# Performance work log

Hardware: AMD Instinct MI355X
Metric: run time of the kernel (lower is better)

## Reference

```python
import jax, jax.numpy as jnp
import numpy as np

# AdaptiveSoftmax.forward (fairseq), no adaptive_inputs, dropout=0 (eval-equivalent).
# cutoff after __init__ appends vocab_size: [10000, 30000, 50000]
CUTOFF = (10000, 30000, 50000)


def setup_inputs() -> dict:
    key = jax.random.key(0)
    ks = jax.random.split(key, 7)
    B, T, D = 2, 2048, 1024
    head_dim = CUTOFF[0] + (len(CUTOFF) - 1)  # 10002
    d0 = int(D // 4.0 ** 1)  # 256
    d1 = int(D // 4.0 ** 2)  # 64
    inp = {
        "input": jax.random.normal(ks[0], (B, T, D), jnp.float32),
        "target": jax.random.randint(ks[1], (B, T), 0, CUTOFF[-1], jnp.int32),
        # xavier-ish scaled params
        "head_w": jax.random.normal(ks[2], (head_dim, D), jnp.float32) * 0.02,
        "proj0_w": jax.random.normal(ks[3], (d0, D), jnp.float32) * 0.04,
        "out0_w": jax.random.normal(ks[4], (CUTOFF[1] - CUTOFF[0], d0), jnp.float32) * 0.02,
        "proj1_w": jax.random.normal(ks[5], (d1, D), jnp.float32) * 0.06,
        "out1_w": jax.random.normal(ks[6], (CUTOFF[2] - CUTOFF[1], d1), jnp.float32) * 0.02,
    }
    return inp


def reference(input, target, head_w, proj0_w, out0_w, proj1_w, out1_w):
    c0, c1, c2 = CUTOFF
    D = input.shape[-1]
    h = input.reshape(-1, D)            # [N, D] (dropout p=0 -> identity)
    t = target.reshape(-1)              # [N]

    # band membership masks (adapt_target routing)
    m0 = (t >= c0) & (t < c1)
    m1 = (t >= c1) & (t < c2)

    # new_target[0]: tail tokens remapped to class slots c0+i
    new_t_head = jnp.where(m0, c0, jnp.where(m1, c0 + 1, t))
    # per-band relative targets (0 for rows not in the band; original returns
    # ragged gathered targets -- here dense+masked equivalent)
    new_t0 = jnp.where(m0, t - c0, 0)
    new_t1 = jnp.where(m1, t - c1, 0)

    # head: Linear(D -> c0 + n_tails, bias=False)
    head_out = jnp.einsum('nd,vd->nv', h, head_w)  # [N, 10002]

    # tails: proj (D->dim) then out (dim->band_size); original applies only to
    # gathered band rows -- dense version masked to zero outside the band
    # computes the same values on band rows.
    tail0 = jnp.einsum('nk,vk->nv', jnp.einsum('nd,kd->nk', h, proj0_w), out0_w)
    tail0 = tail0 * m0[:, None].astype(tail0.dtype)  # [N, 20000]
    tail1 = jnp.einsum('nk,vk->nv', jnp.einsum('nd,kd->nk', h, proj1_w), out1_w)
    tail1 = tail1 * m1[:, None].astype(tail1.dtype)  # [N, 20000]

    return (head_out, tail0, tail1, new_t_head, new_t0, new_t1)
```

## Files before the change

kernel.cpp:

```cpp
#include <hip/hip_runtime.h>

#define C0 10000
#define C1 30000
#define C2 50000

typedef __attribute__((ext_vector_type(8))) short short8;
typedef __attribute__((ext_vector_type(8))) unsigned short ushort8;
typedef __attribute__((ext_vector_type(4))) float f32x4;

__device__ __forceinline__ unsigned short f2bf(float f) {
    unsigned int u = __float_as_uint(f);
    u += 0x7FFF + ((u >> 16) & 1);
    return (unsigned short)(u >> 16);
}

#define SZ_IN    (4096 * 1024)
#define OFF_IN   0
#define HW_ROWSP 10240
#define SZ_HW    (HW_ROWSP * 1024)
#define REAL_HW  (10002 * 1024)
#define OFF_HW   (OFF_IN + SZ_IN)
#define OFF_PJ   (OFF_HW + SZ_HW)
#define SZ_PJ    (512 * 1024)
#define PJ_P0    (256 * 1024)
#define PJ_P1    (64 * 1024)
#define O0_ROWSP 20096
#define SZ_O0    (O0_ROWSP * 256)
#define REAL_O0  (20000 * 256)
#define OFF_O0   (OFF_PJ + SZ_PJ)
#define O1_ROWSP 20096
#define SZ_O1    (O1_ROWSP * 64)
#define REAL_O1  (20000 * 64)
#define OFF_O1   (OFF_O0 + SZ_O0)
#define CVT_TOTAL (OFF_O1 + SZ_O1)
#define OFF_PP0C CVT_TOTAL
#define SZ_PP0C  (4096 * 256)
#define OFF_PP1C (OFF_PP0C + SZ_PP0C)
#define SZ_PP1C  (4096 * 64)
#define OFF_IDX  (OFF_PP1C + SZ_PP1C)

__global__ __launch_bounds__(256) void convert_kernel(
    const float* __restrict__ in,  const float* __restrict__ hw,
    const float* __restrict__ p0w, const float* __restrict__ o0w,
    const float* __restrict__ p1w, const float* __restrict__ o1w,
    unsigned short* __restrict__ ws,
    const int* __restrict__ target,
    float* __restrict__ o3, float* __restrict__ o4, float* __restrict__ o5)
{
    long long tid = (long long)blockIdx.x * blockDim.x + threadIdx.x;
    if (tid < 4096) {
        int tg = target[tid];
        bool m0 = (tg >= C0) && (tg < C1);
        bool m1 = (tg >= C1) && (tg < C2);
        o3[tid] = (float)(m0 ? C0 : (m1 ? (C0 + 1) : tg));
        o4[tid] = (float)(m0 ? (tg - C0) : 0);
        o5[tid] = (float)(m1 ? (tg - C1) : 0);
    }
    long long i = tid * 8;
    if (i >= CVT_TOTAL) return;
    const float* src;
    long long rel, real;
    if (i < OFF_HW)                      { src = in;  rel = i - OFF_IN;            real = SZ_IN;   }
    else if (i < OFF_PJ)                 { src = hw;  rel = i - OFF_HW;            real = REAL_HW; }
    else if (i < OFF_PJ + PJ_P0)         { src = p0w; rel = i - OFF_PJ;            real = PJ_P0;   }
    else if (i < OFF_PJ + PJ_P0 + PJ_P1) { src = p1w; rel = i - (OFF_PJ + PJ_P0);  real = PJ_P1;   }
    else if (i < OFF_O0)                 { src = p1w; rel = 1;                     real = 0;       }
    else if (i < OFF_O1)                 { src = o0w; rel = i - OFF_O0;            real = REAL_O0; }
    else                                 { src = o1w; rel = i - OFF_O1;            real = REAL_O1; }
    ushort8 o;
    if (rel < real) {
        float4 v0 = *(const float4*)(src + rel);
        float4 v1 = *(const float4*)(src + rel + 4);
        o[0] = f2bf(v0.x); o[1] = f2bf(v0.y); o[2] = f2bf(v0.z); o[3] = f2bf(v0.w);
        o[4] = f2bf(v1.x); o[5] = f2bf(v1.y); o[6] = f2bf(v1.z); o[7] = f2bf(v1.w);
    } else {
        o = (ushort8)0;
    }
    *(ushort8*)(ws + i) = o;
}

__global__ __launch_bounds__(1024) void build_idx(const int* __restrict__ target,
                                                  int* __restrict__ idx0,
                                                  int* __restrict__ idx1,
                                                  int* __restrict__ cnts)
{
    __shared__ int wsum0[16], wsum1[16];
    __shared__ int base0, base1;
    const int t = threadIdx.x, lane = t & 63, wv = t >> 6;
    if (t == 0) { base0 = 0; base1 = 0; }
    __syncthreads();
    for (int r = 0; r < 4; r++) {
        int i = r * 1024 + t;
        int tg = target[i];
        bool p0 = (tg >= C0) && (tg < C1);
        bool p1 = (tg >= C1) && (tg < C2);
        unsigned long long b0 = __ballot(p0);
        unsigned long long b1 = __ballot(p1);
        int pre0 = __popcll(b0 & ((1ull << lane) - 1));
        int pre1 = __popcll(b1 & ((1ull << lane) - 1));
        if (lane == 0) { wsum0[wv] = __popcll(b0); wsum1[wv] = __popcll(b1); }
        __syncthreads();
        int woff0 = base0, woff1 = base1;
        for (int k = 0; k < wv; k++) { woff0 += wsum0[k]; woff1 += wsum1[k]; }
        if (p0) idx0[woff0 + pre0] = i;
        if (p1) idx1[woff1 + pre1] = i;
        __syncthreads();
        if (t == 0) {
            for (int k = 0; k < 16; k++) { base0 += wsum0[k]; base1 += wsum1[k]; }
        }
        __syncthreads();
    }
    for (int j = base0 + t; j < 4096; j += 1024) idx0[j] = 0;
    for (int j = base1 + t; j < 4096; j += 1024) idx1[j] = 0;
    if (t == 0) { cnts[0] = base0; cnts[1] = base1; }
}

__global__ __launch_bounds__(256) void fill_nonband(
    const int* __restrict__ target,
    float* __restrict__ tail0, float* __restrict__ tail1)
{
    int row   = blockIdx.x >> 1;
    int which = blockIdx.x & 1;
    int tg = target[row];
    bool in = which ? (tg >= C1 && tg < C2) : (tg >= C0 && tg < C1);
    if (in) return;
    float4* dst = (float4*)((which ? tail1 : tail0) + (size_t)row * 20000);
    float4 z = {0.f, 0.f, 0.f, 0.f};
    for (int i = threadIdx.x; i < 5000; i += 256) dst[i] = z;
}

#define BM 128
#define BN 128
#define BK 64

__global__ __launch_bounds__(256) void proj_gather(
    const unsigned short* __restrict__ A,
    const unsigned short* __restrict__ pjw,
    unsigned short* __restrict__ pp0c, unsigned short* __restrict__ pp1c,
    const int* __restrict__ idx0, const int* __restrict__ idx1,
    const int* __restrict__ cnts)
{
    const int band = blockIdx.z;
    if (band == 1 && blockIdx.x > 0) return;
    const int* idx = band ? idx1 : idx0;
    const int cnt = cnts[band];
    const int mBase = blockIdx.y * BM;
    if (mBase >= cnt) return;
    const unsigned short* B = pjw + (band ? (size_t)PJ_P0 : 0);
    const int Nn = band ? 64 : 256;
    unsigned short* Cb = band ? pp1c : pp0c;
    const int K = 1024;

    __shared__ unsigned short As[BM * BK];
    __shared__ unsigned short Bs[BN * BK];

    const int t    = threadIdx.x;
    const int lane = t & 63;
    const int w    = t >> 6;
    const int wr   = w >> 1;
    const int wc   = w & 1;
    const int nBase = blockIdx.x * BN;
    const int srow = lane >> 3;
    const int scol = (lane & 7) * 8;

    int rowsIdx[4];
    #pragma unroll
    for (int c = 0; c < 4; c++)
        rowsIdx[c] = idx[mBase + w * 32 + c * 8 + srow];

    f32x4 acc[4][4] = {};

    for (int k0 = 0; k0 < K; k0 += BK) {
        #pragma unroll
        for (int c = 0; c < 4; c++) {
            const int rbase = w * 32 + c * 8;
            const unsigned short* ga = A + (size_t)rowsIdx[c] * K + k0 + scol;
            __builtin_amdgcn_global_load_lds(
                (const __attribute__((address_space(1))) void*)ga,
                (__attribute__((address_space(3))) void*)&As[rbase * BK], 16, 0, 0);
            const unsigned short* gb = B + (size_t)(nBase + rbase + srow) * K + k0 + scol;
            __builtin_amdgcn_global_load_lds(
                (const __attribute__((address_space(1))) void*)gb,
                (__attribute__((address_space(3))) void*)&Bs[rbase * BK], 16, 0, 0);
        }
        __syncthreads();

        #pragma unroll
        for (int kk = 0; kk < BK / 32; kk++) {
            const int kOff = kk * 32 + (lane >> 4) * 8;
            short8 a4[4], b4[4];
            #pragma unroll
            for (int m = 0; m < 4; m++)
                a4[m] = *(const short8*)(&As[(wr * 64 + m * 16 + (lane & 15)) * BK + kOff]);
            #pragma unroll
            for (int n = 0; n < 4; n++)
                b4[n] = *(const short8*)(&Bs[(wc * 64 + n * 16 + (lane & 15)) * BK + kOff]);
            #pragma unroll
            for (int m = 0; m < 4; m++)
                #pragma unroll
                for (int n = 0; n < 4; n++)
                    acc[m][n] = __builtin_amdgcn_mfma_f32_16x16x32_bf16(
                        a4[m], b4[n], acc[m][n], 0, 0, 0);
        }
        __syncthreads();
    }

    #pragma unroll
    for (int m = 0; m < 4; m++)
        #pragma unroll
        for (int i = 0; i < 4; i++) {
            int grow = mBase + wr * 64 + m * 16 + (lane >> 4) * 4 + i;
            #pragma unroll
            for (int n = 0; n < 4; n++) {
                int gcol = nBase + wc * 64 + n * 16 + (lane & 15);
                if (gcol < Nn)
                    Cb[(size_t)grow * Nn + gcol] = f2bf(acc[m][n][i]);
            }
        }
}


__device__ __forceinline__ short8 ldsw(const unsigned short* base, int row, int chunk) {
    int slot = chunk ^ (row & 7);
    return *(const short8*)(base + row * 64 + slot * 8);
}

#define STG(dstElemOff, srcPtr)                                                \
  __builtin_amdgcn_global_load_lds(                                            \
      (const __attribute__((address_space(1))) void*)(srcPtr),                 \
      (__attribute__((address_space(3))) void*)(lds + (dstElemOff)), 16, 0, 0);

#define STAGE_A(bf, h, kofs) {                                                 \
    STG((bf)*32768 + (h)*8192 + (w * 8) * 64,        pA[h] + (kofs));          \
    STG((bf)*32768 + (h)*8192 + (64 + w * 8) * 64,   pA[h] + (size_t)64 * K + (kofs)); }
#define STAGE_B(bf, h, kofs) {                                                 \
    STG((bf)*32768 + 16384 + (h)*8192 + (w * 8) * 64,      pB[h] + (kofs));    \
    STG((bf)*32768 + 16384 + (h)*8192 + (64 + w * 8) * 64, pB[h] + (size_t)64 * K + (kofs)); }

#define VM4()  asm volatile("s_waitcnt vmcnt(4)" ::: "memory")
#define BARF() { __builtin_amdgcn_s_barrier(); asm volatile("" ::: "memory"); }

__global__ __launch_bounds__(512) void gemm256(
    const unsigned short* __restrict__ A,
    const unsigned short* __restrict__ B,
    float* __restrict__ C, int Nn, int K, int NT)
{
    __shared__ unsigned short lds[65536];

    const int t    = threadIdx.x;
    const int lane = t & 63;
    const int w    = t >> 6;
    const int wm   = w >> 2;
    const int wn   = w & 3;
    const int lr   = lane & 15;
    const int lq   = lane >> 4;
    const int lr3  = lane >> 3;
    const int swzc = ((lane & 7) ^ lr3) * 8;

    const int swz = (blockIdx.x & 7) * 80 + (blockIdx.x >> 3);
    const int bx = swz >> 4;
    const int by = swz & 15;
    const int mBase = by * 256;
    const int nBase = bx * 256;

    const unsigned short* pA[2];
    const unsigned short* pB[2];
    #pragma unroll
    for (int h = 0; h < 2; h++) {
        pA[h] = A + (size_t)(mBase + h * 128 + w * 8 + lr3) * K + swzc;
        pB[h] = B + (size_t)(nBase + h * 128 + w * 8 + lr3) * K + swzc;
    }

    f32x4 acc[8][4] = {};
    short8 af[4][2], bf0[2][2], bf1[2][2];

    STAGE_A(0, 0, 0); STAGE_B(0, 0, 0); STAGE_B(0, 1, 0); STAGE_A(0, 1, 0);

    for (int kt = 0; kt < NT; ++kt) {
        const int cb = kt & 1, nb2 = cb ^ 1;
        const int kofs = (kt + 1) * 64;
        const unsigned short* Ab0 = lds + cb * 32768;
        const unsigned short* Ab1 = Ab0 + 8192;
        const unsigned short* Bb0 = Ab0 + 16384;
        const unsigned short* Bb1 = Ab0 + 24576;

        VM4(); BARF();
        #pragma unroll
        for (int m = 0; m < 4; m++)
            #pragma unroll
            for (int ks = 0; ks < 2; ks++)
                af[m][ks] = ldsw(Ab0, wm * 64 + m * 16 + lr, ks * 4 + lq);
        #pragma unroll
        for (int n = 0; n < 2; n++)
            #pragma unroll
            for (int ks = 0; ks < 2; ks++)
                bf0[n][ks] = ldsw(Bb0, wn * 32 + n * 16 + lr, ks * 4 + lq);
        STAGE_A(nb2, 0, kofs);
        __builtin_amdgcn_s_setprio(1);
        #pragma unroll
        for (int m = 0; m < 4; m++)
            #pragma unroll
            for (int n = 0; n < 2; n++)
                #pragma unroll
                for (int ks = 0; ks < 2; ks++)
                    acc[m][n] = __builtin_amdgcn_mfma_f32_16x16x32_bf16(
                        af[m][ks], bf0[n][ks], acc[m][n], 0, 0, 0);
        __builtin_amdgcn_s_setprio(0);

        VM4(); BARF();
        #pragma unroll
        for (int n = 0; n < 2; n++)
            #pragma unroll
            for (int ks = 0; ks < 2; ks++)
                bf1[n][ks] = ldsw(Bb1, wn * 32 + n * 16 + lr, ks * 4 + lq);
        STAGE_B(nb2, 0, kofs);
        __builtin_amdgcn_s_setprio(1);
        #pragma unroll
        for (int m = 0; m < 4; m++)
            #pragma unroll
            for (int n = 0; n < 2; n++)
                #pragma unroll
                for (int ks = 0; ks < 2; ks++)
                    acc[m][2 + n] = __builtin_amdgcn_mfma_f32_16x16x32_bf16(
                        af[m][ks], bf1[n][ks], acc[m][2 + n], 0, 0, 0);
        __builtin_amdgcn_s_setprio(0);

        VM4(); BARF();
        #pragma unroll
        for (int m = 0; m < 4; m++)
            #pragma unroll
            for (int ks = 0; ks < 2; ks++)
                af[m][ks] = ldsw(Ab1, wm * 64 + m * 16 + lr, ks * 4 + lq);
        STAGE_B(nb2, 1, kofs);
        __builtin_amdgcn_s_setprio(1);
        #pragma unroll
        for (int m = 0; m < 4; m++)
            #pragma unroll
            for (int n = 0; n < 2; n++)
                #pragma unroll
                for (int ks = 0; ks < 2; ks++)
                    acc[4 + m][2 + n] = __builtin_amdgcn_mfma_f32_16x16x32_bf16(
                        af[m][ks], bf1[n][ks], acc[4 + m][2 + n], 0, 0, 0);
        __builtin_amdgcn_s_setprio(0);

        BARF();
        STAGE_A(nb2, 1, kofs);
        __builtin_amdgcn_s_setprio(1);
        #pragma unroll
        for (int m = 0; m < 4; m++)
            #pragma unroll
            for (int n = 0; n < 2; n++)
                #pragma unroll
                for (int ks = 0; ks < 2; ks++)
                    acc[4 + m][n] = __builtin_amdgcn_mfma_f32_16x16x32_bf16(
                        af[m][ks], bf0[n][ks], acc[4 + m][n], 0, 0, 0);
        __builtin_amdgcn_s_setprio(0);
    }

    #pragma unroll
    for (int m = 0; m < 8; m++) {
        const int growb = mBase + (m >> 2) * 128 + wm * 64 + (m & 3) * 16 + lq * 4;
        #pragma unroll
        for (int i = 0; i < 4; i++) {
            #pragma unroll
            for (int n = 0; n < 4; n++) {
                int gcol = nBase + (n >> 1) * 128 + wn * 32 + (n & 1) * 16 + lr;
                if (gcol < Nn)
                    C[(size_t)(growb + i) * Nn + gcol] = acc[m][n][i];
            }
        }
    }
}

__global__ __launch_bounds__(256) void tails_kernel(
    const unsigned short* __restrict__ pp0c, const unsigned short* __restrict__ pp1c,
    const unsigned short* __restrict__ o0w,  const unsigned short* __restrict__ o1w,
    float* __restrict__ tail0, float* __restrict__ tail1,
    const int* __restrict__ idx0, const int* __restrict__ idx1,
    const int* __restrict__ cnts)
{
    const bool band1 = blockIdx.x >= (O0_ROWSP / BN);
    const int  nb    = band1 ? blockIdx.x - (O0_ROWSP / BN) : blockIdx.x;
    const unsigned short* A = band1 ? pp1c : pp0c;
    const unsigned short* B = band1 ? o1w  : o0w;
    float* Out = band1 ? tail1 : tail0;
    const int* idx = band1 ? idx1 : idx0;
    const int cnt  = cnts[band1 ? 1 : 0];
    const int K    = band1 ? 64 : 256;

    const int mBase = blockIdx.y * BM;
    if (mBase >= cnt) return;

    __shared__ unsigned short As[BM * BK];
    __shared__ unsigned short Bs[BN * BK];

    const int t    = threadIdx.x;
    const int lane = t & 63;
    const int w    = t >> 6;
    const int wr   = w >> 1;
    const int wc   = w & 1;
    const int nBase = nb * BN;
    const int srow = lane >> 3;
    const int scol = (lane & 7) * 8;

    f32x4 acc[4][4] = {};

    for (int k0 = 0; k0 < K; k0 += BK) {
        #pragma unroll
        for (int c = 0; c < 4; c++) {
            const int rbase = w * 32 + c * 8;
            const unsigned short* ga = A + (size_t)(mBase + rbase + srow) * K + k0 + scol;
            __builtin_amdgcn_global_load_lds(
                (const __attribute__((address_space(1))) void*)ga,
                (__attribute__((address_space(3))) void*)&As[rbase * BK], 16, 0, 0);
            const unsigned short* gb = B + (size_t)(nBase + rbase + srow) * K + k0 + scol;
            __builtin_amdgcn_global_load_lds(
                (const __attribute__((address_space(1))) void*)gb,
                (__attribute__((address_space(3))) void*)&Bs[rbase * BK], 16, 0, 0);
        }
        __syncthreads();

        #pragma unroll
        for (int kk = 0; kk < BK / 32; kk++) {
            const int kOff = kk * 32 + (lane >> 4) * 8;
            short8 a4[4], b4[4];
            #pragma unroll
            for (int m = 0; m < 4; m++)
                a4[m] = *(const short8*)(&As[(wr * 64 + m * 16 + (lane & 15)) * BK + kOff]);
            #pragma unroll
            for (int n = 0; n < 4; n++)
                b4[n] = *(const short8*)(&Bs[(wc * 64 + n * 16 + (lane & 15)) * BK + kOff]);
            #pragma unroll
            for (int m = 0; m < 4; m++)
                #pragma unroll
                for (int n = 0; n < 4; n++)
                    acc[m][n] = __builtin_amdgcn_mfma_f32_16x16x32_bf16(
                        a4[m], b4[n], acc[m][n], 0, 0, 0);
        }
        __syncthreads();
    }

    #pragma unroll
    for (int m = 0; m < 4; m++)
        #pragma unroll
        for (int i = 0; i < 4; i++) {
            int grow_local = mBase + wr * 64 + m * 16 + (lane >> 4) * 4 + i;
            if (grow_local < cnt) {
                int gr = idx[grow_local];
                #pragma unroll
                for (int n = 0; n < 4; n++) {
                    int gcol = nBase + wc * 64 + n * 16 + (lane & 15);
                    if (gcol < 20000)
                        Out[(size_t)gr * 20000 + gcol] = acc[m][n][i];
                }
            }
        }
}

extern "C" void kernel_launch(void* const* d_in, const int* in_sizes, int n_in,
                              void* d_out, int out_size, void* d_ws, size_t ws_size,
                              hipStream_t stream)
{
    const float* input   = (const float*)d_in[0];
    const int*   target  = (const int*)  d_in[1];
    const float* head_w  = (const float*)d_in[2];
    const float* proj0_w = (const float*)d_in[3];
    const float* out0_w  = (const float*)d_in[4];
    const float* proj1_w = (const float*)d_in[5];
    const float* out1_w  = (const float*)d_in[6];

    const int N = 4096;

    float* out      = (float*)d_out;
    float* head_out = out;
    float* tail0    = head_out + (size_t)N * 10002;
    float* tail1    = tail0 + (size_t)N * 20000;
    float* o3       = tail1 + (size_t)N * 20000;
    float* o4       = o3 + N;
    float* o5       = o4 + N;

    unsigned short* ws = (unsigned short*)d_ws;
    unsigned short* in_bf  = ws + OFF_IN;
    unsigned short* hw_bf  = ws + OFF_HW;
    unsigned short* pjw_bf = ws + OFF_PJ;
    unsigned short* o0w_bf = ws + OFF_O0;
    unsigned short* o1w_bf = ws + OFF_O1;
    unsigned short* pp0c   = ws + OFF_PP0C;
    unsigned short* pp1c   = ws + OFF_PP1C;
    int* idx0 = (int*)(ws + OFF_IDX);
    int* idx1 = idx0 + 4096;
    int* cnts = idx1 + 4096;

    convert_kernel<<<dim3((CVT_TOTAL / 8 + 255) / 256), dim3(256), 0, stream>>>(
        input, head_w, proj0_w, out0_w, proj1_w, out1_w, ws, target, o3, o4, o5);

    build_idx<<<dim3(1), dim3(1024), 0, stream>>>(target, idx0, idx1, cnts);

    proj_gather<<<dim3(2, N / BM, 2), dim3(256), 0, stream>>>(
        in_bf, pjw_bf, pp0c, pp1c, idx0, idx1, cnts);

    gemm256<<<dim3((HW_ROWSP / 256) * (N / 256)), dim3(512), 0, stream>>>(
        in_bf, hw_bf, head_out, 10002, 1024, 1024 / 64);

    fill_nonband<<<dim3(2 * N), dim3(256), 0, stream>>>(target, tail0, tail1);

    tails_kernel<<<dim3(O0_ROWSP / BN + O1_ROWSP / BN, N / BM), dim3(256), 0, stream>>>(
        pp0c, pp1c, o0w_bf, o1w_bf, tail0, tail1, idx0, idx1, cnts);
}
```

Baseline: 357.7 us.

## Fuse non-band zero fill into tails GEMM kernel with interleaved block scheduling

Merges the separate zero-fill kernel for non-band tail rows into the tails GEMM launch, interleaving 5 GEMM tiles with 4 fill rows per group of 9 blocks. This removes one launch and lets store-bound zero writes overlap with compute-bound GEMM tiles across the GPU. The GEMM tiles are now spread over a 1-D grid with many early-exit blocks. Those idle blocks add scheduling overhead, and the shared memory declaration now also applies to fill blocks, which may lower occupancy for them.

```diff
diff --git a/kernel.cpp b/kernel.cpp
--- a/kernel.cpp
+++ b/kernel.cpp
@@ -115,20 +115,6 @@
     if (t == 0) { cnts[0] = base0; cnts[1] = base1; }
 }
 
-__global__ __launch_bounds__(256) void fill_nonband(
-    const int* __restrict__ target,
-    float* __restrict__ tail0, float* __restrict__ tail1)
-{
-    int row   = blockIdx.x >> 1;
-    int which = blockIdx.x & 1;
-    int tg = target[row];
-    bool in = which ? (tg >= C1 && tg < C2) : (tg >= C0 && tg < C1);
-    if (in) return;
-    float4* dst = (float4*)((which ? tail1 : tail0) + (size_t)row * 20000);
-    float4 z = {0.f, 0.f, 0.f, 0.f};
-    for (int i = threadIdx.x; i < 5000; i += 256) dst[i] = z;
-}
-
 #define BM 128
 #define BN 128
 #define BK 64
@@ -219,7 +205,6 @@
         }
 }
 
-
 __device__ __forceinline__ short8 ldsw(const unsigned short* base, int row, int chunk) {
     int slot = chunk ^ (row & 7);
     return *(const short8*)(base + row * 64 + slot * 8);
@@ -372,15 +357,43 @@
     }
 }
 
-__global__ __launch_bounds__(256) void tails_kernel(
+#define FB 157
+#define NTAIL (FB * 32)
+#define NGROUP 2048
+
+__global__ __launch_bounds__(256) void tails_fill(
     const unsigned short* __restrict__ pp0c, const unsigned short* __restrict__ pp1c,
     const unsigned short* __restrict__ o0w,  const unsigned short* __restrict__ o1w,
     float* __restrict__ tail0, float* __restrict__ tail1,
     const int* __restrict__ idx0, const int* __restrict__ idx1,
-    const int* __restrict__ cnts)
+    const int* __restrict__ cnts, const int* __restrict__ target)
 {
-    const bool band1 = blockIdx.x >= (O0_ROWSP / BN);
-    const int  nb    = band1 ? blockIdx.x - (O0_ROWSP / BN) : blockIdx.x;
+    __shared__ unsigned short As[BM * BK];
+    __shared__ unsigned short Bs[BN * BK];
+
+    const int G = blockIdx.x / 9;
+    const int r = blockIdx.x % 9;
+
+    if (r >= 5) {
+        int f = G * 4 + (r - 5);
+        int row   = f >> 1;
+        int which = f & 1;
+        int tg = target[row];
+        bool in = which ? (tg >= C1 && tg < C2) : (tg >= C0 && tg < C1);
+        if (in) return;
+        float4* dst = (float4*)((which ? tail1 : tail0) + (size_t)row * 20000);
+        float4 z = {0.f, 0.f, 0.f, 0.f};
+        for (int i = threadIdx.x; i < 5000; i += 256) dst[i] = z;
+        return;
+    }
+
+    int slot = G * 5 + r;
+    if (slot >= 2 * NTAIL) return;
+    const bool band1 = slot >= NTAIL;
+    const int  s     = band1 ? slot - NTAIL : slot;
+    const int  nb    = s % FB;
+    const int  my    = s / FB;
+
     const unsigned short* A = band1 ? pp1c : pp0c;
     const unsigned short* B = band1 ? o1w  : o0w;
     float* Out = band1 ? tail1 : tail0;
@@ -388,11 +401,8 @@
     const int cnt  = cnts[band1 ? 1 : 0];
     const int K    = band1 ? 64 : 256;
 
-    const int mBase = blockIdx.y * BM;
+    const int mBase = my * BM;
     if (mBase >= cnt) return;
-
-    __shared__ unsigned short As[BM * BK];
-    __shared__ unsigned short Bs[BN * BK];
 
     const int t    = threadIdx.x;
     const int lane = t & 63;
@@ -502,8 +512,6 @@
     gemm256<<<dim3((HW_ROWSP / 256) * (N / 256)), dim3(512), 0, stream>>>(
         in_bf, hw_bf, head_out, 10002, 1024, 1024 / 64);
 
-    fill_nonband<<<dim3(2 * N), dim3(256), 0, stream>>>(target, tail0, tail1);
-
-    tails_kernel<<<dim3(O0_ROWSP / BN + O1_ROWSP / BN, N / BM), dim3(256), 0, stream>>>(
-        pp0c, pp1c, o0w_bf, o1w_bf, tail0, tail1, idx0, idx1, cnts);
-}
+    tails_fill<<<dim3(NGROUP * 9), dim3(256), 0, stream>>>(
+        pp0c, pp1c, o0w_bf, o1w_bf, tail0, tail1, idx0, idx1, cnts, target);
+}
```

Measured after the change: 329.8 us. 7.8% less time.

## Fuse head GEMM, tail GEMMs and zero-fill into one persistent-style launch

Applied to the files above, without the earlier changes.

Replaces three launches (head gemm256, fill_nonband, tails_kernel) with a single fused kernel. Head tiles and 256x256 tail tiles are interleaved across the grid: every fifth block does a head tile, the rest do tail tiles, and all blocks share the zero-fill of non-band rows. The tail GEMMs now use the same 256x256 double-buffered MFMA pipeline as the head. The aim is to cut launch gaps and tail-effect idle time, and to overlap the memory-bound fills and stores with compute. In exchange, tail padding grows to 20224 rows, some blocks exit early when beyond the band count, and the fused kernel needs more registers.

```diff
diff --git a/kernel.cpp b/kernel.cpp
--- a/kernel.cpp
+++ b/kernel.cpp
@@ -24,12 +24,11 @@
 #define SZ_PJ    (512 * 1024)
 #define PJ_P0    (256 * 1024)
 #define PJ_P1    (64 * 1024)
-#define O0_ROWSP 20096
-#define SZ_O0    (O0_ROWSP * 256)
+#define O_ROWSP  20224
+#define SZ_O0    (O_ROWSP * 256)
 #define REAL_O0  (20000 * 256)
 #define OFF_O0   (OFF_PJ + SZ_PJ)
-#define O1_ROWSP 20096
-#define SZ_O1    (O1_ROWSP * 64)
+#define SZ_O1    (O_ROWSP * 64)
 #define REAL_O1  (20000 * 64)
 #define OFF_O1   (OFF_O0 + SZ_O0)
 #define CVT_TOTAL (OFF_O1 + SZ_O1)
@@ -115,20 +114,6 @@
     if (t == 0) { cnts[0] = base0; cnts[1] = base1; }
 }
 
-__global__ __launch_bounds__(256) void fill_nonband(
-    const int* __restrict__ target,
-    float* __restrict__ tail0, float* __restrict__ tail1)
-{
-    int row   = blockIdx.x >> 1;
-    int which = blockIdx.x & 1;
-    int tg = target[row];
-    bool in = which ? (tg >= C1 && tg < C2) : (tg >= C0 && tg < C1);
-    if (in) return;
-    float4* dst = (float4*)((which ? tail1 : tail0) + (size_t)row * 20000);
-    float4 z = {0.f, 0.f, 0.f, 0.f};
-    for (int i = threadIdx.x; i < 5000; i += 256) dst[i] = z;
-}
-
 #define BM 128
 #define BN 128
 #define BK 64
@@ -240,13 +225,20 @@
 #define VM4()  asm volatile("s_waitcnt vmcnt(4)" ::: "memory")
 #define BARF() { __builtin_amdgcn_s_barrier(); asm volatile("" ::: "memory"); }
 
-__global__ __launch_bounds__(512) void gemm256(
-    const unsigned short* __restrict__ A,
-    const unsigned short* __restrict__ B,
-    float* __restrict__ C, int Nn, int K, int NT)
+#define NB_FUSED 3200
+#define TAIL_SLOTS 2528
+
+__global__ __launch_bounds__(512) void fused_kernel(
+    const unsigned short* __restrict__ in_bf, const unsigned short* __restrict__ hw_bf,
+    const unsigned short* __restrict__ pp0c,  const unsigned short* __restrict__ pp1c,
+    const unsigned short* __restrict__ o0w,   const unsigned short* __restrict__ o1w,
+    float* __restrict__ head_out, float* __restrict__ tail0, float* __restrict__ tail1,
+    const int* __restrict__ idx0, const int* __restrict__ idx1,
+    const int* __restrict__ cnts, const int* __restrict__ target)
 {
     __shared__ unsigned short lds[65536];
 
+    const int L    = blockIdx.x;
     const int t    = threadIdx.x;
     const int lane = t & 63;
     const int w    = t >> 6;
@@ -257,204 +249,160 @@
     const int lr3  = lane >> 3;
     const int swzc = ((lane & 7) ^ lr3) * 8;
 
-    const int swz = (blockIdx.x & 7) * 80 + (blockIdx.x >> 3);
-    const int bx = swz >> 4;
-    const int by = swz & 15;
-    const int mBase = by * 256;
-    const int nBase = bx * 256;
-
-    const unsigned short* pA[2];
-    const unsigned short* pB[2];
-    #pragma unroll
-    for (int h = 0; h < 2; h++) {
-        pA[h] = A + (size_t)(mBase + h * 128 + w * 8 + lr3) * K + swzc;
-        pB[h] = B + (size_t)(nBase + h * 128 + w * 8 + lr3) * K + swzc;
-    }
-
-    f32x4 acc[8][4] = {};
-    short8 af[4][2], bf0[2][2], bf1[2][2];
-
-    STAGE_A(0, 0, 0); STAGE_B(0, 0, 0); STAGE_B(0, 1, 0); STAGE_A(0, 1, 0);
-
-    for (int kt = 0; kt < NT; ++kt) {
-        const int cb = kt & 1, nb2 = cb ^ 1;
-        const int kofs = (kt + 1) * 64;
-        const unsigned short* Ab0 = lds + cb * 32768;
-        const unsigned short* Ab1 = Ab0 + 8192;
-        const unsigned short* Bb0 = Ab0 + 16384;
-        const unsigned short* Bb1 = Ab0 + 24576;
-
-        VM4(); BARF();
+    const unsigned short *A = nullptr, *B = nullptr;
+    float* Cp = nullptr;
+    const int* idx = nullptr;
+    int K = 0, NT = 0, Nn = 0, Mlimit = 0, mBase = 0, nBase = 0;
+    bool live = false;
+
+    if (L % 5 == 0) {
+        int h = L / 5;
+        int swz = (h & 7) * 80 + (h >> 3);
+        nBase = (swz >> 4) * 256;
+        mBase = (swz & 15) * 256;
+        A = in_bf; B = hw_bf; Cp = head_out;
+        K = 1024; NT = 16; Nn = 10002; Mlimit = 4096;
+        live = true;
+    } else {
+        int s = L - L / 5 - 1;
+        if (s < TAIL_SLOTS) {
+            int band = s / 1264;
+            int r    = s % 1264;
+            nBase = (r / 16) * 256;
+            mBase = (r % 16) * 256;
+            if (band == 0) { A = pp0c; B = o0w; Cp = tail0; idx = idx0; K = 256; NT = 4; }
+            else           { A = pp1c; B = o1w; Cp = tail1; idx = idx1; K = 64;  NT = 1; }
+            Nn = 20000;
+            Mlimit = cnts[band];
+            live = (mBase < Mlimit);
+        }
+    }
+
+    if (live) {
+        const unsigned short* pA[2];
+        const unsigned short* pB[2];
         #pragma unroll
-        for (int m = 0; m < 4; m++)
-            #pragma unroll
-            for (int ks = 0; ks < 2; ks++)
-                af[m][ks] = ldsw(Ab0, wm * 64 + m * 16 + lr, ks * 4 + lq);
+        for (int h = 0; h < 2; h++) {
+            pA[h] = A + (size_t)(mBase + h * 128 + w * 8 + lr3) * K + swzc;
+            pB[h] = B + (size_t)(nBase + h * 128 + w * 8 + lr3) * K + swzc;
+        }
+
+        f32x4 acc[8][4] = {};
+        short8 af[4][2], bf0[2][2], bf1[2][2];
+
+        STAGE_A(0, 0, 0); STAGE_B(0, 0, 0); STAGE_B(0, 1, 0); STAGE_A(0, 1, 0);
+
+        for (int kt = 0; kt < NT; ++kt) {
+            const int cb = kt & 1, nb2 = cb ^ 1;
+            const int kofs = (kt + 1) * 64;
+            const unsigned short* Ab0 = lds + cb * 32768;
+            const unsigned short* Ab1 = Ab0 + 8192;
+            const unsigned short* Bb0 = Ab0 + 16384;
+            const unsigned short* Bb1 = Ab0 + 24576;
+
+            VM4(); BARF();
+            #pragma unroll
+            for (int m = 0; m < 4; m++)
+                #pragma unroll
+                for (int ks = 0; ks < 2; ks++)
+                    af[m][ks] = ldsw(Ab0, wm * 64 + m * 16 + lr, ks * 4 + lq);
+            #pragma unroll
+            for (int n = 0; n < 2; n++)
+                #pragma unroll
+                for (int ks = 0; ks < 2; ks++)
+                    bf0[n][ks] = ldsw(Bb0, wn * 32 + n * 16 + lr, ks * 4 + lq);
+            STAGE_A(nb2, 0, kofs);
+            __builtin_amdgcn_s_setprio(1);
+            #pragma unroll
+            for (int m = 0; m < 4; m++)
+                #pragma unroll
+                for (int n = 0; n < 2; n++)
+                    #pragma unroll
+                    for (int ks = 0; ks < 2; ks++)
+                        acc[m][n] = __builtin_amdgcn_mfma_f32_16x16x32_bf16(
+                            af[m][ks], bf0[n][ks], acc[m][n], 0, 0, 0);
+            __builtin_amdgcn_s_setprio(0);
+
+            VM4(); BARF();
+            #pragma unroll
+            for (int n = 0; n < 2; n++)
+                #pragma unroll
+                for (int ks = 0; ks < 2; ks++)
+                    bf1[n][ks] = ldsw(Bb1, wn * 32 + n * 16 + lr, ks * 4 + lq);
+            STAGE_B(nb2, 0, kofs);
+            __builtin_amdgcn_s_setprio(1);
+            #pragma unroll
+            for (int m = 0; m < 4; m++)
+                #pragma unroll
+                for (int n = 0; n < 2; n++)
+                    #pragma unroll
+                    for (int ks = 0; ks < 2; ks++)
+                        acc[m][2 + n] = __builtin_amdgcn_mfma_f32_16x16x32_bf16(
+                            af[m][ks], bf1[n][ks], acc[m][2 + n], 0, 0, 0);
+            __builtin_amdgcn_s_setprio(0);
+
+            VM4(); BARF();
+            #pragma unroll
+            for (int m = 0; m < 4; m++)
+                #pragma unroll
+                for (int ks = 0; ks < 2; ks++)
+                    af[m][ks] = ldsw(Ab1, wm * 64 + m * 16 + lr, ks * 4 + lq);
+            STAGE_B(nb2, 1, kofs);
+            __builtin_amdgcn_s_setprio(1);
+            #pragma unroll
+            for (int m = 0; m < 4; m++)
+                #pragma unroll
+                for (int n = 0; n < 2; n++)
+                    #pragma unroll
+                    for (int ks = 0; ks < 2; ks++)
+                        acc[4 + m][2 + n] = __builtin_amdgcn_mfma_f32_16x16x32_bf16(
+                            af[m][ks], bf1[n][ks], acc[4 + m][2 + n], 0, 0, 0);
+            __builtin_amdgcn_s_setprio(0);
+
+            BARF();
+            STAGE_A(nb2, 1, kofs);
+            __builtin_amdgcn_s_setprio(1);
+            #pragma unroll
+            for (int m = 0; m < 4; m++)
+                #pragma unroll
+                for (int n = 0; n < 2; n++)
+                    #pragma unroll
+                    for (int ks = 0; ks < 2; ks++)
+                        acc[4 + m][n] = __builtin_amdgcn_mfma_f32_16x16x32_bf16(
+                            af[m][ks], bf0[n][ks], acc[4 + m][n], 0, 0, 0);
+            __builtin_amdgcn_s_setprio(0);
+        }
+
         #pragma unroll
-        for (int n = 0; n < 2; n++)
-            #pragma unroll
-            for (int ks = 0; ks < 2; ks++)
-                bf0[n][ks] = ldsw(Bb0, wn * 32 + n * 16 + lr, ks * 4 + lq);
-        STAGE_A(nb2, 0, kofs);
-        __builtin_amdgcn_s_setprio(1);
-        #pragma unroll
-        for (int m = 0; m < 4; m++)
-            #pragma unroll
-            for (int n = 0; n < 2; n++)
-                #pragma unroll
-                for (int ks = 0; ks < 2; ks++)
-                    acc[m][n] = __builtin_amdgcn_mfma_f32_16x16x32_bf16(
-                        af[m][ks], bf0[n][ks], acc[m][n], 0, 0, 0);
-        __builtin_amdgcn_s_setprio(0);
-
-        VM4(); BARF();
-        #pragma unroll
-        for (int n = 0; n < 2; n++)
-            #pragma unroll
-            for (int ks = 0; ks < 2; ks++)
-                bf1[n][ks] = ldsw(Bb1, wn * 32 + n * 16 + lr, ks * 4 + lq);
-        STAGE_B(nb2, 0, kofs);
-        __builtin_amdgcn_s_setprio(1);
-        #pragma unroll
-        for (int m = 0; m < 4; m++)
-            #pragma unroll
-            for (int n = 0; n < 2; n++)
-                #pragma unroll
-                for (int ks = 0; ks < 2; ks++)
-                    acc[m][2 + n] = __builtin_amdgcn_mfma_f32_16x16x32_bf16(
-                        af[m][ks], bf1[n][ks], acc[m][2 + n], 0, 0, 0);
-        __builtin_amdgcn_s_setprio(0);
-
-        VM4(); BARF();
-        #pragma unroll
-        for (int m = 0; m < 4; m++)
-            #pragma unroll
-            for (int ks = 0; ks < 2; ks++)
-                af[m][ks] = ldsw(Ab1, wm * 64 + m * 16 + lr, ks * 4 + lq);
-        STAGE_B(nb2, 1, kofs);
-        __builtin_amdgcn_s_setprio(1);
-        #pragma unroll
-        for (int m = 0; m < 4; m++)
-            #pragma unroll
-            for (int n = 0; n < 2; n++)
-                #pragma unroll
-                for (int ks = 0; ks < 2; ks++)
-                    acc[4 + m][2 + n] = __builtin_amdgcn_mfma_f32_16x16x32_bf16(
-                        af[m][ks], bf1[n][ks], acc[4 + m][2 + n], 0, 0, 0);
-        __builtin_amdgcn_s_setprio(0);
-
-        BARF();
-        STAGE_A(nb2, 1, kofs);
-        __builtin_amdgcn_s_setprio(1);
-        #pragma unroll
-        for (int m = 0; m < 4; m++)
-            #pragma unroll
-            for (int n = 0; n < 2; n++)
-                #pragma unroll
-                for (int ks = 0; ks < 2; ks++)
-                    acc[4 + m][n] = __builtin_amdgcn_mfma_f32_16x16x32_bf16(
-                        af[m][ks], bf0[n][ks], acc[4 + m][n], 0, 0, 0);
-        __builtin_amdgcn_s_setprio(0);
-    }
-
-    #pragma unroll
-    for (int m = 0; m < 8; m++) {
-        const int growb = mBase + (m >> 2) * 128 + wm * 64 + (m & 3) * 16 + lq * 4;
-        #pragma unroll
-        for (int i = 0; i < 4; i++) {
-            #pragma unroll
-            for (int n = 0; n < 4; n++) {
-                int gcol = nBase + (n >> 1) * 128 + wn * 32 + (n & 1) * 16 + lr;
-                if (gcol < Nn)
-                    C[(size_t)(growb + i) * Nn + gcol] = acc[m][n][i];
-            }
-        }
-    }
-}
-
-__global__ __launch_bounds__(256) void tails_kernel(
-    const unsigned short* __restrict__ pp0c, const unsigned short* __restrict__ pp1c,
-    const unsigned short* __restrict__ o0w,  const unsigned short* __restrict__ o1w,
-    float* __restrict__ tail0, float* __restrict__ tail1,
-    const int* __restrict__ idx0, const int* __restrict__ idx1,
-    const int* __restrict__ cnts)
-{
-    const bool band1 = blockIdx.x >= (O0_ROWSP / BN);
-    const int  nb    = band1 ? blockIdx.x - (O0_ROWSP / BN) : blockIdx.x;
-    const unsigned short* A = band1 ? pp1c : pp0c;
-    const unsigned short* B = band1 ? o1w  : o0w;
-    float* Out = band1 ? tail1 : tail0;
-    const int* idx = band1 ? idx1 : idx0;
-    const int cnt  = cnts[band1 ? 1 : 0];
-    const int K    = band1 ? 64 : 256;
-
-    const int mBase = blockIdx.y * BM;
-    if (mBase >= cnt) return;
-
-    __shared__ unsigned short As[BM * BK];
-    __shared__ unsigned short Bs[BN * BK];
-
-    const int t    = threadIdx.x;
-    const int lane = t & 63;
-    const int w    = t >> 6;
-    const int wr   = w >> 1;
-    const int wc   = w & 1;
-    const int nBase = nb * BN;
-    const int srow = lane >> 3;
-    const int scol = (lane & 7) * 8;
-
-    f32x4 acc[4][4] = {};
-
-    for (int k0 = 0; k0 < K; k0 += BK) {
-        #pragma unroll
-        for (int c = 0; c < 4; c++) {
-            const int rbase = w * 32 + c * 8;
-            const unsigned short* ga = A + (size_t)(mBase + rbase + srow) * K + k0 + scol;
-            __builtin_amdgcn_global_load_lds(
-                (const __attribute__((address_space(1))) void*)ga,
-                (__attribute__((address_space(3))) void*)&As[rbase * BK], 16, 0, 0);
-            const unsigned short* gb = B + (size_t)(nBase + rbase + srow) * K + k0 + scol;
-            __builtin_amdgcn_global_load_lds(
-                (const __attribute__((address_space(1))) void*)gb,
-                (__attribute__((address_space(3))) void*)&Bs[rbase * BK], 16, 0, 0);
-        }
-        __syncthreads();
-
-        #pragma unroll
-        for (int kk = 0; kk < BK / 32; kk++) {
-            const int kOff = kk * 32 + (lane >> 4) * 8;
-            short8 a4[4], b4[4];
-            #pragma unroll
-            for (int m = 0; m < 4; m++)
-                a4[m] = *(const short8*)(&As[(wr * 64 + m * 16 + (lane & 15)) * BK + kOff]);
-            #pragma unroll
-            for (int n = 0; n < 4; n++)
-                b4[n] = *(const short8*)(&Bs[(wc * 64 + n * 16 + (lane & 15)) * BK + kOff]);
-            #pragma unroll
-            for (int m = 0; m < 4; m++)
-                #pragma unroll
-                for (int n = 0; n < 4; n++)
-                    acc[m][n] = __builtin_amdgcn_mfma_f32_16x16x32_bf16(
-                        a4[m], b4[n], acc[m][n], 0, 0, 0);
-        }
-        __syncthreads();
-    }
-
-    #pragma unroll
-    for (int m = 0; m < 4; m++)
-        #pragma unroll
-        for (int i = 0; i < 4; i++) {
-            int grow_local = mBase + wr * 64 + m * 16 + (lane >> 4) * 4 + i;
-            if (grow_local < cnt) {
-                int gr = idx[grow_local];
-                #pragma unroll
-                for (int n = 0; n < 4; n++) {
-                    int gcol = nBase + wc * 64 + n * 16 + (lane & 15);
-                    if (gcol < 20000)
-                        Out[(size_t)gr * 20000 + gcol] = acc[m][n][i];
+        for (int m = 0; m < 8; m++) {
+            const int growb = mBase + (m >> 2) * 128 + wm * 64 + (m & 3) * 16 + lq * 4;
+            #pragma unroll
+            for (int i = 0; i < 4; i++) {
+                int grow = growb + i;
+                if (grow < Mlimit) {
+                    int gr = idx ? idx[grow] : grow;
+                    #pragma unroll
+                    for (int n = 0; n < 4; n++) {
+                        int gcol = nBase + (n >> 1) * 128 + wn * 32 + (n & 1) * 16 + lr;
+                        if (gcol < Nn)
+                            Cp[(size_t)gr * Nn + gcol] = acc[m][n][i];
+                    }
                 }
             }
         }
+    }
+
+    for (int j = L; j < 8192; j += NB_FUSED) {
+        int row   = j >> 1;
+        int which = j & 1;
+        int tg = target[row];
+        bool in = which ? (tg >= C1 && tg < C2) : (tg >= C0 && tg < C1);
+        if (!in) {
+            float4* dst = (float4*)((which ? tail1 : tail0) + (size_t)row * 20000);
+            float4 z = {0.f, 0.f, 0.f, 0.f};
+            for (int q = t; q < 5000; q += 512) dst[q] = z;
+        }
+    }
 }
 
 extern "C" void kernel_launch(void* const* d_in, const int* in_sizes, int n_in,
@@ -499,11 +447,7 @@
     proj_gather<<<dim3(2, N / BM, 2), dim3(256), 0, stream>>>(
         in_bf, pjw_bf, pp0c, pp1c, idx0, idx1, cnts);
 
-    gemm256<<<dim3((HW_ROWSP / 256) * (N / 256)), dim3(512), 0, stream>>>(
-        in_bf, hw_bf, head_out, 10002, 1024, 1024 / 64);
-
-    fill_nonband<<<dim3(2 * N), dim3(256), 0, stream>>>(target, tail0, tail1);
-
-    tails_kernel<<<dim3(O0_ROWSP / BN + O1_ROWSP / BN, N / BM), dim3(256), 0, stream>>>(
-        pp0c, pp1c, o0w_bf, o1w_bf, tail0, tail1, idx0, idx1, cnts);
-}
+    fused_kernel<<<dim3(NB_FUSED), dim3(512), 0, stream>>>(
+        in_bf, hw_bf, pp0c, pp1c, o0w_bf, o1w_bf,
+        head_out, tail0, tail1, idx0, idx1, cnts, target);
+}
```

New measurement: 322.4 us. 9.9% less time.
